# Optimization experiments

Measured on AMD Instinct MI355X. Metric: run time of the kernel, lower is better.

Reference implementation:

```python
import jax, jax.numpy as jnp
import numpy as np

IN_FEATURES = 4096
OUT_FEATURES = 11008
B, S = 8, 512


def setup_inputs() -> dict:
    key = jax.random.key(0)
    k1, k2, k3 = jax.random.split(key, 3)
    x = jax.random.normal(k1, (B, S, IN_FEATURES), dtype=jnp.float32)
    # int8 weights simulated as int32 values in [-127, 127]
    weight_int8 = jax.random.randint(k2, (OUT_FEATURES, IN_FEATURES), -127, 128, dtype=jnp.int32)
    # per-output-channel scales (positive, small, like absmax/127)
    weight_scale = jax.random.uniform(k3, (OUT_FEATURES,), dtype=jnp.float32) * 0.01 + 1e-4
    return {"x": x, "weight_int8": weight_int8, "weight_scale": weight_scale}


def reference(x, weight_int8, weight_scale):
    # On-the-fly dequantization: W[o, i] = int8[o, i] * scale[o]
    weight = weight_int8.astype(x.dtype) * weight_scale.astype(x.dtype)[:, None]
    # F.linear: y = x @ W^T  -> [B, S, out_features]
    return jnp.einsum('bsi,oi->bso', x, weight)
```

## Files before the change

kernel.cpp:

```cpp
#include <hip/hip_runtime.h>
#include <stdint.h>

#define M_DIM 4096
#define N_DIM 11008
#define K_DIM 4096

typedef int i32x4 __attribute__((ext_vector_type(4)));

static __device__ __forceinline__ void direct_load16(const void* gptr, void* ldsptr) {
    __builtin_amdgcn_global_load_lds(
        (const __attribute__((address_space(1))) void*)gptr,
        (__attribute__((address_space(3))) void*)ldsptr,
        16, 0, 0);
}

__global__ __launch_bounds__(256) void cvt_w_kernel(const int* __restrict__ w,
                                                    int8_t* __restrict__ o) {
    int t = blockIdx.x * 256 + threadIdx.x;
    const int4* w4 = (const int4*)w;
    int4 a = w4[t];
    ((unsigned*)o)[t] = (a.x & 255) | ((a.y & 255) << 8) | ((a.z & 255) << 16) | (a.w << 24);
}

__global__ __launch_bounds__(256) void quant_x_kernel(const float* __restrict__ x,
                                                      int8_t* __restrict__ xq,
                                                      float* __restrict__ xs) {
    __shared__ float wmax[4];
    const int row = blockIdx.x;
    const int t = threadIdx.x;
    const float4* xr = (const float4*)(x + (size_t)row * K_DIM);

    float4 v[4];
    float am = 0.0f;
#pragma unroll
    for (int p = 0; p < 4; p++) {
        v[p] = xr[p * 256 + t];
        am = fmaxf(am, fmaxf(fmaxf(fabsf(v[p].x), fabsf(v[p].y)),
                             fmaxf(fabsf(v[p].z), fabsf(v[p].w))));
    }
#pragma unroll
    for (int o = 32; o > 0; o >>= 1)
        am = fmaxf(am, __shfl_xor(am, o));
    if ((t & 63) == 0) wmax[t >> 6] = am;
    __syncthreads();
    am = fmaxf(fmaxf(wmax[0], wmax[1]), fmaxf(wmax[2], wmax[3]));

    const float inv = 127.0f / am;
    int* oq = (int*)(xq + (size_t)row * K_DIM);
#pragma unroll
    for (int p = 0; p < 4; p++) {
        int qa = (int)rintf(v[p].x * inv);
        int qb = (int)rintf(v[p].y * inv);
        int qc = (int)rintf(v[p].z * inv);
        int qd = (int)rintf(v[p].w * inv);
        oq[p * 256 + t] = (qa & 255) | ((qb & 255) << 8) | ((qc & 255) << 16) | (qd << 24);
    }
    if (t == 0) xs[row] = am * (1.0f / 127.0f);
}


__global__ __launch_bounds__(512, 2) void gemm_i8_kernel(
    const int8_t* __restrict__ A,
    const int8_t* __restrict__ B,
    const float* __restrict__ xs,
    const float* __restrict__ ws,
    float* __restrict__ C)
{
    __shared__ __align__(16) int8_t As[4][256 * 64];
    __shared__ __align__(16) int8_t Bs[4][256 * 64];

    const int tid  = threadIdx.x;
    const int lane = tid & 63;
    const int wave = tid >> 6;
    const int wm   = wave >> 2;
    const int wn   = wave & 3;
    const int quad = lane >> 4;
    const int r16  = lane & 15;

    const int orig = blockIdx.x + (blockIdx.y << 4);
    const int work = (orig & 7) * 86 + (orig >> 3);
    const int m0 = (work & 15) * 256;
    const int n0 = (work >> 4) * 256;

    const int srow   = tid >> 2;
    const int schunk = (tid & 3) ^ ((tid >> 3) & 3);
    const int8_t* gA = A + (size_t)(m0 + srow) * K_DIM + schunk * 16;
    const int8_t* gB = B + (size_t)(n0 + srow) * K_DIM + schunk * 16;
    const size_t half2 = (size_t)128 * K_DIM;
    const int wb = wave * 1024;

    const int fsw   = (r16 >> 1) & 3;
    const int a_off = (wm * 128 + r16) * 64 + ((quad ^ fsw) * 16);
    const int b_off = (wn * 64  + r16) * 64 + ((quad ^ fsw) * 16);

    i32x4 acc[8][4];
#pragma unroll
    for (int i = 0; i < 8; i++)
#pragma unroll
        for (int j = 0; j < 4; j++) acc[i][j] = (i32x4)(0);

#define STAGE_A(t, buf) do {                                                  \
        direct_load16(gA + (size_t)(t) * 64,         (char*)As[buf] + wb);    \
        direct_load16(gA + (size_t)(t) * 64 + half2, (char*)As[buf] + wb + 8192); \
    } while (0)
#define STAGE_B(t, buf) do {                                                  \
        direct_load16(gB + (size_t)(t) * 64,         (char*)Bs[buf] + wb);    \
        direct_load16(gB + (size_t)(t) * 64 + half2, (char*)Bs[buf] + wb + 8192); \
    } while (0)

#define PHASE(rbuf, h, STAGE_STMT, DOVM) do {                                 \
        const int8_t* _as = As[rbuf];                                         \
        const int8_t* _bs = Bs[rbuf];                                         \
        i32x4 af[4], bf[4];                                                   \
        _Pragma("unroll")                                                     \
        for (int _i = 0; _i < 4; _i++)                                        \
            af[_i] = *(const i32x4*)(_as + a_off + ((h) * 4 + _i) * 1024);    \
        _Pragma("unroll")                                                     \
        for (int _j = 0; _j < 4; _j++)                                        \
            bf[_j] = *(const i32x4*)(_bs + b_off + _j * 1024);                \
        STAGE_STMT;                                                           \
        __builtin_amdgcn_s_barrier();                                         \
        __builtin_amdgcn_s_setprio(1);                                        \
        _Pragma("unroll")                                                     \
        for (int _i = 0; _i < 4; _i++)                                        \
            _Pragma("unroll")                                                 \
            for (int _j = 0; _j < 4; _j++)                                    \
                acc[(h) * 4 + _i][_j] = __builtin_amdgcn_mfma_i32_16x16x64_i8(\
                    af[_i], bf[_j], acc[(h) * 4 + _i][_j], 0, 0, 0);          \
        __builtin_amdgcn_s_setprio(0);                                        \
        if (DOVM) asm volatile("s_waitcnt vmcnt(8)" ::: "memory");            \
        __builtin_amdgcn_s_barrier();                                         \
    } while (0)

    STAGE_A(0, 0); STAGE_B(0, 0);
    STAGE_A(1, 1); STAGE_B(1, 1);
    STAGE_A(2, 2); STAGE_B(2, 2);
    asm volatile("s_waitcnt vmcnt(8)" ::: "memory");
    __builtin_amdgcn_s_barrier();

    for (int i = 0; i < 16; ++i) {
        const int t3 = 4 * i + 3;
        const int t4 = (4 * i + 4 > 63) ? 63 : 4 * i + 4;
        const int t5 = (4 * i + 5 > 63) ? 63 : 4 * i + 5;
        const int t6 = (4 * i + 6 > 63) ? 63 : 4 * i + 6;
        PHASE(0, 0, STAGE_A(t3, 3), 0);
        PHASE(0, 1, STAGE_B(t3, 3), 1);
        PHASE(1, 0, STAGE_A(t4, 0), 0);
        PHASE(1, 1, STAGE_B(t4, 0), 1);
        PHASE(2, 0, STAGE_A(t5, 1), 0);
        PHASE(2, 1, STAGE_B(t5, 1), 1);
        PHASE(3, 0, STAGE_A(t6, 2), 0);
        PHASE(3, 1, STAGE_B(t6, 2), 1);
    }

#undef PHASE
#undef STAGE_A
#undef STAGE_B

#pragma unroll
    for (int i = 0; i < 8; i++) {
        const int mrow = m0 + wm * 128 + i * 16 + quad * 4;
        float rsc[4];
#pragma unroll
        for (int r = 0; r < 4; r++) rsc[r] = xs[mrow + r];
#pragma unroll
        for (int j = 0; j < 4; j++) {
            const int n = n0 + wn * 64 + j * 16 + r16;
            const float s = ws[n];
#pragma unroll
            for (int r = 0; r < 4; r++)
                C[(size_t)(mrow + r) * N_DIM + n] = (float)acc[i][j][r] * s * rsc[r];
        }
    }
}


extern "C" void kernel_launch(void* const* d_in, const int* in_sizes, int n_in,
                              void* d_out, int out_size, void* d_ws, size_t ws_size,
                              hipStream_t stream) {
    const float* x       = (const float*)d_in[0];
    const int*   w_int   = (const int*)d_in[1];
    const float* w_scale = (const float*)d_in[2];
    float*       out     = (float*)d_out;

    int8_t* wq = (int8_t*)d_ws;
    int8_t* xq = (int8_t*)((char*)d_ws + (size_t)N_DIM * K_DIM);
    float*  xs = (float*)((char*)d_ws + (size_t)N_DIM * K_DIM + (size_t)M_DIM * K_DIM);

    cvt_w_kernel<<<dim3(N_DIM * K_DIM / 4 / 256), dim3(256), 0, stream>>>(w_int, wq);
    quant_x_kernel<<<dim3(M_DIM), dim3(256), 0, stream>>>(x, xq, xs);
    gemm_i8_kernel<<<dim3(M_DIM / 256, N_DIM / 256), dim3(512), 0, stream>>>(xq, wq, xs, w_scale, out);
}
```

Measured before the change: 555.6 us.

## Double-buffer LDS fragments in registers and drop a barrier per phase

Reorganizes the int8 GEMM main loop so each phase loads the next A and B MFMA fragments from LDS into a second register set while the current MFMAs run. This removes the barrier that separated fragment loads from compute in each phase. The global-to-LDS wait becomes vmcnt(4) after every phase instead of vmcnt(8) after every other phase. The extra fragment registers raise register pressure under the 512-thread, two-blocks-per-CU launch bound, which can cause spills, and the reduced synchronization makes buffer-reuse correctness more delicate.

```diff
diff --git a/kernel.cpp b/kernel.cpp
--- a/kernel.cpp
+++ b/kernel.cpp
@@ -99,6 +99,8 @@
 #pragma unroll
         for (int j = 0; j < 4; j++) acc[i][j] = (i32x4)(0);
 
+    i32x4 afX[4], afY[4], bfA[4], bfB[4];
+
 #define STAGE_A(t, buf) do {                                                  \
         direct_load16(gA + (size_t)(t) * 64,         (char*)As[buf] + wb);    \
         direct_load16(gA + (size_t)(t) * 64 + half2, (char*)As[buf] + wb + 8192); \
@@ -108,54 +110,57 @@
         direct_load16(gB + (size_t)(t) * 64 + half2, (char*)Bs[buf] + wb + 8192); \
     } while (0)
 
-#define PHASE(rbuf, h, STAGE_STMT, DOVM) do {                                 \
-        const int8_t* _as = As[rbuf];                                         \
-        const int8_t* _bs = Bs[rbuf];                                         \
-        i32x4 af[4], bf[4];                                                   \
+#define LDA4(dst, buf, fb) do {                                               \
+        const int8_t* _p = As[buf];                                           \
         _Pragma("unroll")                                                     \
         for (int _i = 0; _i < 4; _i++)                                        \
-            af[_i] = *(const i32x4*)(_as + a_off + ((h) * 4 + _i) * 1024);    \
-        _Pragma("unroll")                                                     \
-        for (int _j = 0; _j < 4; _j++)                                        \
-            bf[_j] = *(const i32x4*)(_bs + b_off + _j * 1024);                \
-        STAGE_STMT;                                                           \
-        __builtin_amdgcn_s_barrier();                                         \
+            dst[_i] = *(const i32x4*)(_p + a_off + ((fb) + _i) * 1024);       \
+    } while (0)
+#define LDB2(dst, buf, j0) do {                                               \
+        const int8_t* _p = Bs[buf];                                           \
+        dst[(j0)]     = *(const i32x4*)(_p + b_off + ((j0)) * 1024);          \
+        dst[(j0) + 1] = *(const i32x4*)(_p + b_off + ((j0) + 1) * 1024);      \
+    } while (0)
+#define MM(AF, BF, H) do {                                                    \
         __builtin_amdgcn_s_setprio(1);                                        \
         _Pragma("unroll")                                                     \
         for (int _i = 0; _i < 4; _i++)                                        \
             _Pragma("unroll")                                                 \
             for (int _j = 0; _j < 4; _j++)                                    \
-                acc[(h) * 4 + _i][_j] = __builtin_amdgcn_mfma_i32_16x16x64_i8(\
-                    af[_i], bf[_j], acc[(h) * 4 + _i][_j], 0, 0, 0);          \
+                acc[(H) * 4 + _i][_j] = __builtin_amdgcn_mfma_i32_16x16x64_i8(\
+                    AF[_i], BF[_j], acc[(H) * 4 + _i][_j], 0, 0, 0);          \
         __builtin_amdgcn_s_setprio(0);                                        \
-        if (DOVM) asm volatile("s_waitcnt vmcnt(8)" ::: "memory");            \
+        asm volatile("s_waitcnt vmcnt(4)" ::: "memory");                      \
         __builtin_amdgcn_s_barrier();                                         \
     } while (0)
 
     STAGE_A(0, 0); STAGE_B(0, 0);
     STAGE_A(1, 1); STAGE_B(1, 1);
     STAGE_A(2, 2); STAGE_B(2, 2);
-    asm volatile("s_waitcnt vmcnt(8)" ::: "memory");
+    asm volatile("s_waitcnt vmcnt(4)" ::: "memory");
     __builtin_amdgcn_s_barrier();
 
-    for (int i = 0; i < 16; ++i) {
-        const int t3 = 4 * i + 3;
-        const int t4 = (4 * i + 4 > 63) ? 63 : 4 * i + 4;
-        const int t5 = (4 * i + 5 > 63) ? 63 : 4 * i + 5;
-        const int t6 = (4 * i + 6 > 63) ? 63 : 4 * i + 6;
-        PHASE(0, 0, STAGE_A(t3, 3), 0);
-        PHASE(0, 1, STAGE_B(t3, 3), 1);
-        PHASE(1, 0, STAGE_A(t4, 0), 0);
-        PHASE(1, 1, STAGE_B(t4, 0), 1);
-        PHASE(2, 0, STAGE_A(t5, 1), 0);
-        PHASE(2, 1, STAGE_B(t5, 1), 1);
-        PHASE(3, 0, STAGE_A(t6, 2), 0);
-        PHASE(3, 1, STAGE_B(t6, 2), 1);
+    LDA4(afX, 0, 0);
+    LDB2(bfA, 0, 0); LDB2(bfA, 0, 2);
+
+    for (int u = 0; u < 32; ++u) {
+        const int t0 = 2 * u, t1 = t0 + 1;
+        const int b0 = t0 & 3, b1 = t1 & 3, b2 = (t0 + 2) & 3;
+        const int sb0 = (t0 + 3) & 3, sb1 = (t0 + 4) & 3;
+        const int s0 = (t0 + 3 > 63) ? 63 : t0 + 3;
+        const int s1 = (t0 + 4 > 63) ? 63 : t0 + 4;
+
+        LDA4(afY, b0, 4); LDB2(bfB, b1, 0); STAGE_A(s0, sb0); MM(afX, bfA, 0);
+        LDA4(afX, b1, 0); LDB2(bfB, b1, 2); STAGE_B(s0, sb0); MM(afY, bfA, 1);
+        LDA4(afY, b1, 4); LDB2(bfA, b2, 0); STAGE_A(s1, sb1); MM(afX, bfB, 0);
+        LDA4(afX, b2, 0); LDB2(bfA, b2, 2); STAGE_B(s1, sb1); MM(afY, bfB, 1);
     }
 
-#undef PHASE
+#undef MM
+#undef LDB2
+#undef LDA4
+#undef STAGE_B
 #undef STAGE_A
-#undef STAGE_B
 
 #pragma unroll
     for (int i = 0; i < 8; i++) {
```

Result: faster. 542.0 us (-2.5%).

## Collapse two half-phases per K-tile into one phase with a single barrier

Applied to the files above, without the earlier changes.

The main loop drops the two half-phases per K-tile, each of which had two barriers. Each iteration now reads all 8 A fragments and 4 B fragments from LDS, issues the prefetch for tile t+3, runs 32 MFMAs, then waits and hits one barrier. This cuts barrier count per tile from four to one and stops reading the B fragments twice per tile. The cost is more live fragment registers, which adds register pressure and a possible spill risk under the 2-blocks-per-CU bound. It also gives coarser interleaving of LDS reads, global prefetch and MFMA work across waves.

```diff
diff --git a/kernel.cpp b/kernel.cpp
--- a/kernel.cpp
+++ b/kernel.cpp
@@ -108,54 +108,46 @@
         direct_load16(gB + (size_t)(t) * 64 + half2, (char*)Bs[buf] + wb + 8192); \
     } while (0)
 
-#define PHASE(rbuf, h, STAGE_STMT, DOVM) do {                                 \
-        const int8_t* _as = As[rbuf];                                         \
-        const int8_t* _bs = Bs[rbuf];                                         \
-        i32x4 af[4], bf[4];                                                   \
-        _Pragma("unroll")                                                     \
-        for (int _i = 0; _i < 4; _i++)                                        \
-            af[_i] = *(const i32x4*)(_as + a_off + ((h) * 4 + _i) * 1024);    \
-        _Pragma("unroll")                                                     \
-        for (int _j = 0; _j < 4; _j++)                                        \
-            bf[_j] = *(const i32x4*)(_bs + b_off + _j * 1024);                \
-        STAGE_STMT;                                                           \
-        __builtin_amdgcn_s_barrier();                                         \
-        __builtin_amdgcn_s_setprio(1);                                        \
-        _Pragma("unroll")                                                     \
-        for (int _i = 0; _i < 4; _i++)                                        \
-            _Pragma("unroll")                                                 \
-            for (int _j = 0; _j < 4; _j++)                                    \
-                acc[(h) * 4 + _i][_j] = __builtin_amdgcn_mfma_i32_16x16x64_i8(\
-                    af[_i], bf[_j], acc[(h) * 4 + _i][_j], 0, 0, 0);          \
-        __builtin_amdgcn_s_setprio(0);                                        \
-        if (DOVM) asm volatile("s_waitcnt vmcnt(8)" ::: "memory");            \
-        __builtin_amdgcn_s_barrier();                                         \
-    } while (0)
-
     STAGE_A(0, 0); STAGE_B(0, 0);
     STAGE_A(1, 1); STAGE_B(1, 1);
     STAGE_A(2, 2); STAGE_B(2, 2);
     asm volatile("s_waitcnt vmcnt(8)" ::: "memory");
     __builtin_amdgcn_s_barrier();
 
-    for (int i = 0; i < 16; ++i) {
-        const int t3 = 4 * i + 3;
-        const int t4 = (4 * i + 4 > 63) ? 63 : 4 * i + 4;
-        const int t5 = (4 * i + 5 > 63) ? 63 : 4 * i + 5;
-        const int t6 = (4 * i + 6 > 63) ? 63 : 4 * i + 6;
-        PHASE(0, 0, STAGE_A(t3, 3), 0);
-        PHASE(0, 1, STAGE_B(t3, 3), 1);
-        PHASE(1, 0, STAGE_A(t4, 0), 0);
-        PHASE(1, 1, STAGE_B(t4, 0), 1);
-        PHASE(2, 0, STAGE_A(t5, 1), 0);
-        PHASE(2, 1, STAGE_B(t5, 1), 1);
-        PHASE(3, 0, STAGE_A(t6, 2), 0);
-        PHASE(3, 1, STAGE_B(t6, 2), 1);
+    for (int t = 0; t < 64; ++t) {
+        const int b  = t & 3;
+        const int sb = (t + 3) & 3;
+        const int s  = (t + 3 > 63) ? 63 : t + 3;
+
+        const int8_t* as = As[b];
+        const int8_t* bs = Bs[b];
+        i32x4 bf[4];
+#pragma unroll
+        for (int j = 0; j < 4; j++)
+            bf[j] = *(const i32x4*)(bs + b_off + j * 1024);
+        i32x4 af[8];
+#pragma unroll
+        for (int i = 0; i < 8; i++)
+            af[i] = *(const i32x4*)(as + a_off + i * 1024);
+
+        STAGE_A(s, sb);
+        STAGE_B(s, sb);
+
+        __builtin_amdgcn_s_setprio(1);
+#pragma unroll
+        for (int i = 0; i < 8; i++)
+#pragma unroll
+            for (int j = 0; j < 4; j++)
+                acc[i][j] = __builtin_amdgcn_mfma_i32_16x16x64_i8(
+                    af[i], bf[j], acc[i][j], 0, 0, 0);
+        __builtin_amdgcn_s_setprio(0);
+
+        asm volatile("s_waitcnt vmcnt(8)" ::: "memory");
+        __builtin_amdgcn_s_barrier();
     }
 
-#undef PHASE
+#undef STAGE_B
 #undef STAGE_A
-#undef STAGE_B
 
 #pragma unroll
     for (int i = 0; i < 8; i++) {
@@ -166,10 +158,10 @@
 #pragma unroll
         for (int j = 0; j < 4; j++) {
             const int n = n0 + wn * 64 + j * 16 + r16;
-            const float s = ws[n];
+            const float sc = ws[n];
 #pragma unroll
             for (int r = 0; r < 4; r++)
-                C[(size_t)(mrow + r) * N_DIM + n] = (float)acc[i][j][r] * s * rsc[r];
+                C[(size_t)(mrow + r) * N_DIM + n] = (float)acc[i][j][r] * sc * rsc[r];
         }
     }
 }
```

Measured after the change: 545.3 us. Within noise of the previous version (-1.9%).
